# Performance work log

Hardware: AMD Instinct MI355X
Metric: run time of the kernel (lower is better)

Reference implementation:

```python
import jax, jax.numpy as jnp
import numpy as np

N, P, T, D = 25000, 100000, 4, 128
DIN = 4 * D + 4  # 516
LEAKY = 0.001


def setup_inputs() -> dict:
    key = jax.random.key(0)
    ks = jax.random.split(key, 12)
    inp = {
        "coords": jax.random.normal(ks[0], (N, T, 3), jnp.float32),
        "propers": jax.random.randint(ks[1], (P, 4), 0, N, jnp.int64),
        "encoded": jax.random.normal(ks[2], (N, D), jnp.float32),
        "t": jax.random.uniform(ks[3], (T,), jnp.float32),
        "answer": jax.random.normal(ks[4], (N, T, 3), jnp.float32),
        # AggregateMLP(516 -> 128 -> 128 -> 128 -> 2), LeakyReLU(0.001) between
        "W0": jax.random.normal(ks[5], (DIN, D), jnp.float32) / np.sqrt(DIN),
        "b0": jnp.zeros((D,), jnp.float32),
        "W1": jax.random.normal(ks[6], (D, D), jnp.float32) / np.sqrt(D),
        "b1": jnp.zeros((D,), jnp.float32),
        "W2": jax.random.normal(ks[7], (D, D), jnp.float32) / np.sqrt(D),
        "b2": jnp.zeros((D,), jnp.float32),
        "W3": jax.random.normal(ks[8], (D, 2), jnp.float32) / np.sqrt(D),
        "b3": jnp.zeros((2,), jnp.float32),
    }
    return inp


def _forward(coords, propers, encoded, t, answer, W0, b0, W1, b1, W2, b2, W3, b3):
    p0, p1, p2, p3 = propers[:, 0], propers[:, 1], propers[:, 2], propers[:, 3]
    c0, c1, c2, c3 = coords[p0], coords[p1], coords[p2], coords[p3]  # [P,T,3]
    u1 = c1 - c0
    u2 = c2 - c1
    u3 = c3 - c2
    u1xu2 = jnp.cross(u1, u2, axis=-1)
    u2xu3 = jnp.cross(u2, u3, axis=-1)
    u2_norm = jnp.linalg.norm(u2, axis=-1, keepdims=True)
    u1yu2 = u1 * u2_norm
    theta = jnp.arctan2((u1yu2 * u2xu3).sum(-1), (u1xu2 * u2xu3).sum(-1))  # [P,T]
    dr = c0 - c3  # [P,T,3]
    dl = jnp.sqrt(jnp.clip(jnp.square(dr).sum(-1), 1e-12))  # [P,T]
    dh = dr / dl[..., None]

    Pn, Tn = propers.shape[0], t.shape[0]
    bcast = lambda e: jnp.broadcast_to(e[:, None, :], (Pn, Tn, e.shape[-1]))
    feats = jnp.concatenate(
        [
            bcast(encoded[p0]),
            bcast(encoded[p1]),
            bcast(encoded[p2]),
            bcast(encoded[p3]),
            jnp.broadcast_to(t.reshape(1, Tn, 1), (Pn, Tn, 1)),
            jnp.sin(theta)[..., None],
            jnp.cos(theta)[..., None],
            dl[..., None],
        ],
        axis=2,
    )  # [P,T,516]

    h = jax.nn.leaky_relu(feats @ W0 + b0, LEAKY)
    h = jax.nn.leaky_relu(h @ W1 + b1, LEAKY)
    h = jax.nn.leaky_relu(h @ W2 + b2, LEAKY)
    delta = h @ W3 + b3  # [P,T,2]

    out = answer.at[p0].add(-0.5 * delta[:, :, 0:1] * dh)
    out = out.at[p3].add(0.5 * delta[:, :, 1:2] * dh)
    return out


def reference(coords, propers, encoded, t, answer, W0, b0, W1, b1, W2, b2, W3, b3):
    return _forward(coords, propers, encoded, t, answer, W0, b0, W1, b1, W2, b2, W3, b3)
```

## Files before the change

### kernel.cpp

```cpp
#include <hip/hip_runtime.h>
#include <hip/hip_bf16.h>

#define NN 25000
#define PP 100000
#define TT 4
#define DD 128
#define LEAKY 0.001f

#define PB 32
#define ROWS 128

typedef __bf16 bf16;
typedef __bf16 bf16x8 __attribute__((ext_vector_type(8)));
typedef float  f32x4  __attribute__((ext_vector_type(4)));

#define OFF_ENCB  0u
#define OFF_W0SW  6400000u
#define OFF_W1SW  6531072u
#define OFF_W2SW  6563840u
#define OFF_W3SW  6596608u
#define WS_END    6600704u

#define PR_ENCB4 800000
#define PR_W0SW  65536
#define PR_W1SW  16384
#define PR_W2SW  16384
#define PR_W3SW  2048
#define PR_COPY4 75000
#define PR_TOTAL (PR_ENCB4 + PR_W0SW + PR_W1SW + PR_W2SW + PR_W3SW + PR_COPY4)

__global__ __launch_bounds__(256) void prep_kernel(
    const float* __restrict__ encoded, const float* __restrict__ W0,
    const float* __restrict__ W1, const float* __restrict__ W2,
    const float* __restrict__ W3, const float* __restrict__ answer,
    bf16* __restrict__ encB, bf16* __restrict__ W0sw, bf16* __restrict__ W1sw,
    bf16* __restrict__ W2sw, bf16* __restrict__ W3sw, float* __restrict__ out)
{
    int idx = blockIdx.x * 256 + threadIdx.x;
    if (idx < PR_ENCB4) {
        float4 v = ((const float4*)encoded)[idx];
        bf16 pk[4] = {(bf16)v.x, (bf16)v.y, (bf16)v.z, (bf16)v.w};
        *(uint2*)(encB + idx * 4) = *(const uint2*)pk;
        return;
    }
    idx -= PR_ENCB4;
    if (idx < PR_W0SW) {
        int j = idx & 7, lane = (idx >> 3) & 63, c = idx >> 9;
        int fr = lane & 15, quad = lane >> 4;
        int kc = c & 15, iwv = c >> 4;
        int k = kc * 32 + quad * 8 + j;
        W0sw[idx] = (bf16)W0[k * 128 + iwv * 16 + fr];
        return;
    }
    idx -= PR_W0SW;
    if (idx < PR_W1SW) {
        int j = idx & 7, lane = (idx >> 3) & 63, c = idx >> 9;
        int fr = lane & 15, quad = lane >> 4;
        int kc = c & 3, nt = c >> 2;
        int k = kc * 32 + quad * 8 + j;
        W1sw[idx] = (bf16)W1[k * 128 + nt * 16 + fr];
        return;
    }
    idx -= PR_W1SW;
    if (idx < PR_W2SW) {
        int j = idx & 7, lane = (idx >> 3) & 63, c = idx >> 9;
        int fr = lane & 15, quad = lane >> 4;
        int kc = c & 3, nt = c >> 2;
        int k = kc * 32 + quad * 8 + j;
        W2sw[idx] = (bf16)W2[k * 128 + nt * 16 + fr];
        return;
    }
    idx -= PR_W2SW;
    if (idx < PR_W3SW) {
        int j = idx & 7, lane = (idx >> 3) & 63, kc = idx >> 9;
        int fr = lane & 15, quad = lane >> 4;
        int k = kc * 32 + quad * 8 + j;
        W3sw[idx] = (fr < 2) ? (bf16)W3[k * 2 + fr] : (bf16)0.0f;
        return;
    }
    idx -= PR_W3SW;
    if (idx < PR_COPY4) { ((float4*)out)[idx] = ((const float4*)answer)[idx]; }
}

__global__ __launch_bounds__(512, 4) void main_kernel(
    const float* __restrict__ coords, const int* __restrict__ propers,
    const float* __restrict__ tvec, const float* __restrict__ W0,
    const float* __restrict__ b0, const float* __restrict__ b1,
    const float* __restrict__ b2, const float* __restrict__ b3,
    const bf16* __restrict__ encB, const bf16* __restrict__ W0sw,
    const bf16* __restrict__ W1sw, const bf16* __restrict__ W2sw,
    const bf16* __restrict__ W3sw, float* __restrict__ out)
{
    __shared__ bf16 sBuf0[ROWS * 136];
    __shared__ bf16 sBuf1[ROWS * 136];
    #define SA(p, c)  sBuf1[(p) * 520 + (c)]
    #define SH0(r, j) sBuf0[(r) * 136 + (j)]
    #define SH1(r, j) sBuf1[(r) * 136 + (j)]
    __shared__ int   sNodes[PB][4];
    __shared__ float sSn[ROWS], sCs[ROWS], sDl[ROWS], sDh[ROWS][3];
    __shared__ float sDelta[ROWS][2];

    const int tid  = threadIdx.x;
    const int pBase = blockIdx.x * PB;
    const float tv0 = tvec[0], tv1 = tvec[1], tv2 = tvec[2], tv3 = tvec[3];

    {
        int row = tid >> 2, sg = tid & 3;
        int p = row >> 2, i = row & 3;
        int node = propers[(pBase + p) * 4 + i];
        if (sg == 0) sNodes[p][i] = node;
        const uint4* src = (const uint4*)(encB + (size_t)node * 128 + sg * 32);
        uint4* dst = (uint4*)(&SA(p, i * 128 + sg * 32));
        #pragma unroll
        for (int q = 0; q < 4; ++q) dst[q] = src[q];
    }
    if (tid < ROWS) {
        int r = tid, p = r >> 2, t = r & 3;
        const int* prow = propers + (pBase + p) * 4;
        int n0 = prow[0], n1 = prow[1], n2 = prow[2], n3 = prow[3];
        const float* c0 = coords + n0 * 12 + t * 3;
        const float* c1 = coords + n1 * 12 + t * 3;
        const float* c2 = coords + n2 * 12 + t * 3;
        const float* c3 = coords + n3 * 12 + t * 3;
        float u1x = c1[0]-c0[0], u1y = c1[1]-c0[1], u1z = c1[2]-c0[2];
        float u2x = c2[0]-c1[0], u2y = c2[1]-c1[1], u2z = c2[2]-c1[2];
        float u3x = c3[0]-c2[0], u3y = c3[1]-c2[1], u3z = c3[2]-c2[2];
        float ax = u1y*u2z - u1z*u2y, ay = u1z*u2x - u1x*u2z, az = u1x*u2y - u1y*u2x;
        float bx = u2y*u3z - u2z*u3y, by = u2z*u3x - u2x*u3z, bz = u2x*u3y - u2y*u3x;
        float u2n = sqrtf(u2x*u2x + u2y*u2y + u2z*u2z);
        float num = u2n * (u1x*bx + u1y*by + u1z*bz);
        float den = ax*bx + ay*by + az*bz;
        float hyp = sqrtf(num*num + den*den);
        float sn, cs;
        if (hyp > 1e-30f) { float ih = 1.0f / hyp; sn = num * ih; cs = den * ih; }
        else { sn = 0.0f; cs = 1.0f; }
        float drx = c0[0]-c3[0], dry = c0[1]-c3[1], drz = c0[2]-c3[2];
        float dl = sqrtf(fmaxf(drx*drx + dry*dry + drz*drz, 1e-12f));
        float il = 1.0f / dl;
        sSn[r] = sn; sCs[r] = cs; sDl[r] = dl;
        sDh[r][0] = drx * il; sDh[r][1] = dry * il; sDh[r][2] = drz * il;
    }
    __syncthreads();

    const int wv = tid >> 6, lane = tid & 63;
    const int fr = lane & 15;
    const int quad = lane >> 4;

    f32x4 acc0 = {0.f,0.f,0.f,0.f}, acc1 = {0.f,0.f,0.f,0.f};
    {
        const bf16* aB0 = &SA(fr, quad * 8);
        const bf16* aB1 = &SA(16 + fr, quad * 8);
        const bf16* w0b = W0sw + (size_t)wv * 16 * 512 + lane * 8;
        #pragma unroll
        for (int kc = 0; kc < 16; ++kc) {
            bf16x8 bF  = *(const bf16x8*)(w0b + kc * 512);
            bf16x8 aF0 = *(const bf16x8*)(aB0 + kc * 32);
            bf16x8 aF1 = *(const bf16x8*)(aB1 + kc * 32);
            acc0 = __builtin_amdgcn_mfma_f32_16x16x32_bf16(aF0, bF, acc0, 0, 0, 0);
            acc1 = __builtin_amdgcn_mfma_f32_16x16x32_bf16(aF1, bF, acc1, 0, 0, 0);
        }
    }
    {
        int j = wv * 16 + fr;
        float w512 = W0[512 * 128 + j], w513 = W0[513 * 128 + j];
        float w514 = W0[514 * 128 + j], w515 = W0[515 * 128 + j];
        float bb = b0[j];
        #pragma unroll
        for (int s = 0; s < 2; ++s) {
            const f32x4 a = s ? acc1 : acc0;
            #pragma unroll
            for (int reg = 0; reg < 4; ++reg) {
                int p = s * 16 + quad * 4 + reg;
                float g = a[reg] + bb;
                #pragma unroll
                for (int t = 0; t < 4; ++t) {
                    int r = p * 4 + t;
                    float tvv = (t == 0) ? tv0 : (t == 1) ? tv1 : (t == 2) ? tv2 : tv3;
                    float v = g + tvv * w512 + sSn[r] * w513 + sCs[r] * w514 + sDl[r] * w515;
                    v = fmaxf(v, LEAKY * v);
                    SH0(r, j) = (bf16)v;
                }
            }
        }
    }
    __syncthreads();

    const int m2 = (wv & 3) * 2;
    const int nh = wv >> 2;

    #pragma unroll
    for (int s = 0; s < 2; ++s) {
        f32x4 hacc[4];
        #pragma unroll
        for (int nt = 0; nt < 4; ++nt) hacc[nt] = (f32x4){0.f,0.f,0.f,0.f};
        const bf16* aRow = &SH0((m2 + s) * 16 + fr, quad * 8);
        const bf16* w1b = W1sw + lane * 8;
        #pragma unroll
        for (int kc = 0; kc < 4; ++kc) {
            bf16x8 aF = *(const bf16x8*)(aRow + kc * 32);
            #pragma unroll
            for (int nt = 0; nt < 4; ++nt) {
                bf16x8 bF = *(const bf16x8*)(w1b + ((nh * 4 + nt) * 4 + kc) * 512);
                hacc[nt] = __builtin_amdgcn_mfma_f32_16x16x32_bf16(aF, bF, hacc[nt], 0, 0, 0);
            }
        }
        #pragma unroll
        for (int nt = 0; nt < 4; ++nt) {
            int j = (nh * 4 + nt) * 16 + fr;
            float bb = b1[j];
            #pragma unroll
            for (int reg = 0; reg < 4; ++reg) {
                int r = (m2 + s) * 16 + quad * 4 + reg;
                float v = hacc[nt][reg] + bb;
                v = fmaxf(v, LEAKY * v);
                SH1(r, j) = (bf16)v;
            }
        }
    }
    __syncthreads();

    #pragma unroll
    for (int s = 0; s < 2; ++s) {
        f32x4 hacc[4];
        #pragma unroll
        for (int nt = 0; nt < 4; ++nt) hacc[nt] = (f32x4){0.f,0.f,0.f,0.f};
        const bf16* aRow = &SH1((m2 + s) * 16 + fr, quad * 8);
        const bf16* w2b = W2sw + lane * 8;
        #pragma unroll
        for (int kc = 0; kc < 4; ++kc) {
            bf16x8 aF = *(const bf16x8*)(aRow + kc * 32);
            #pragma unroll
            for (int nt = 0; nt < 4; ++nt) {
                bf16x8 bF = *(const bf16x8*)(w2b + ((nh * 4 + nt) * 4 + kc) * 512);
                hacc[nt] = __builtin_amdgcn_mfma_f32_16x16x32_bf16(aF, bF, hacc[nt], 0, 0, 0);
            }
        }
        #pragma unroll
        for (int nt = 0; nt < 4; ++nt) {
            int j = (nh * 4 + nt) * 16 + fr;
            float bb = b2[j];
            #pragma unroll
            for (int reg = 0; reg < 4; ++reg) {
                int r = (m2 + s) * 16 + quad * 4 + reg;
                float v = hacc[nt][reg] + bb;
                v = fmaxf(v, LEAKY * v);
                SH0(r, j) = (bf16)v;
            }
        }
    }
    __syncthreads();

    {
        f32x4 dacc = {0.f,0.f,0.f,0.f};
        const bf16* aRow = &SH0(wv * 16 + fr, quad * 8);
        const bf16* w3b = W3sw + lane * 8;
        #pragma unroll
        for (int kc = 0; kc < 4; ++kc) {
            bf16x8 aF = *(const bf16x8*)(aRow + kc * 32);
            bf16x8 bF = *(const bf16x8*)(w3b + kc * 512);
            dacc = __builtin_amdgcn_mfma_f32_16x16x32_bf16(aF, bF, dacc, 0, 0, 0);
        }
        if (fr < 2) {
            float bb = b3[fr];
            #pragma unroll
            for (int reg = 0; reg < 4; ++reg)
                sDelta[wv * 16 + quad * 4 + reg][fr] = dacc[reg] + bb;
        }
    }
    __syncthreads();

    for (int idx = tid; idx < ROWS * 6; idx += 512) {
        int r = idx / 6, c = idx % 6;
        int p = r >> 2, t = r & 3;
        int side = c / 3, ax = c % 3;
        int node = sNodes[p][side ? 3 : 0];
        float dval = side ? 0.5f * sDelta[r][1] : -0.5f * sDelta[r][0];
        atomicAdd(out + node * 12 + t * 3 + ax, dval * sDh[r][ax]);
    }
    #undef SA
    #undef SH0
    #undef SH1
}

extern "C" void kernel_launch(void* const* d_in, const int* in_sizes, int n_in,
                              void* d_out, int out_size, void* d_ws, size_t ws_size,
                              hipStream_t stream) {
    const float* coords  = (const float*)d_in[0];
    const int*   propers = (const int*)d_in[1];
    const float* encoded = (const float*)d_in[2];
    const float* tvec    = (const float*)d_in[3];
    const float* answer  = (const float*)d_in[4];
    const float* W0 = (const float*)d_in[5];
    const float* b0 = (const float*)d_in[6];
    const float* W1 = (const float*)d_in[7];
    const float* b1 = (const float*)d_in[8];
    const float* W2 = (const float*)d_in[9];
    const float* b2 = (const float*)d_in[10];
    const float* W3 = (const float*)d_in[11];
    const float* b3 = (const float*)d_in[12];
    float* out = (float*)d_out;
    char* ws = (char*)d_ws;
    bf16* encB = (bf16*)(ws + OFF_ENCB);
    bf16* W0sw = (bf16*)(ws + OFF_W0SW);
    bf16* W1sw = (bf16*)(ws + OFF_W1SW);
    bf16* W2sw = (bf16*)(ws + OFF_W2SW);
    bf16* W3sw = (bf16*)(ws + OFF_W3SW);

    int prep_blocks = (PR_TOTAL + 255) / 256;
    prep_kernel<<<prep_blocks, 256, 0, stream>>>(encoded, W0, W1, W2, W3, answer,
                                                 encB, W0sw, W1sw, W2sw, W3sw, out);
    main_kernel<<<PP / PB, 512, 0, stream>>>(coords, propers, tvec, W0, b0, b1, b2, b3,
                                             encB, W0sw, W1sw, W2sw, W3sw, out);
}
```

Measured before the change: 206.2 us.

## Precompute per-node first-layer projections and gather them instead of per-proper GEMM

The first MLP layer is linear in the four gathered embeddings, so a new kernel precomputes encoded @ W0 slice for each of the four slots per node (N×4×128 in bf16). The main kernel then gathers and sums four projected rows per proper instead of running a 512-wide K GEMM over 32 propers per block. This removes most of the layer-0 MFMA work, since it is done once per node rather than once per proper. In exchange it adds an extra kernel launch and about 25 MB of workspace writes and reads. It also introduces an extra bf16 rounding of each partial product before summation.

After: 204.9 us. No clear change (-0.6%).

```diff
diff --git a/kernel.cpp b/kernel.cpp
--- a/kernel.cpp
+++ b/kernel.cpp
@@ -19,7 +19,8 @@
 #define OFF_W1SW  6531072u
 #define OFF_W2SW  6563840u
 #define OFF_W3SW  6596608u
-#define WS_END    6600704u
+#define OFF_E     6600704u
+#define WS_END    32200704u
 
 #define PR_ENCB4 800000
 #define PR_W0SW  65536
@@ -82,18 +83,52 @@
     if (idx < PR_COPY4) { ((float4*)out)[idx] = ((const float4*)answer)[idx]; }
 }
 
+__global__ __launch_bounds__(512, 4) void prep_e_kernel(
+    const bf16* __restrict__ encB, const bf16* __restrict__ W0sw,
+    bf16* __restrict__ E)
+{
+    __shared__ bf16 sA[16][136];
+    const int tid = threadIdx.x;
+    const int row0 = blockIdx.x * 16;
+    if (tid < 256) {
+        int row = tid >> 4, seg = tid & 15;
+        int rr = row0 + row; if (rr > NN - 1) rr = NN - 1;
+        *(bf16x8*)(&sA[row][seg * 8]) =
+            *(const bf16x8*)(encB + (size_t)rr * 128 + seg * 8);
+    }
+    __syncthreads();
+    const int wv = tid >> 6, lane = tid & 63;
+    const int fr = lane & 15, quad = lane >> 4;
+    const bf16* aBase = &sA[fr][quad * 8];
+    #pragma unroll
+    for (int i = 0; i < 4; ++i) {
+        f32x4 dacc = {0.f, 0.f, 0.f, 0.f};
+        #pragma unroll
+        for (int kcc = 0; kcc < 4; ++kcc) {
+            bf16x8 aF = *(const bf16x8*)(aBase + kcc * 32);
+            bf16x8 bF = *(const bf16x8*)(W0sw + ((size_t)wv * 16 + i * 4 + kcc) * 512 + lane * 8);
+            dacc = __builtin_amdgcn_mfma_f32_16x16x32_bf16(aF, bF, dacc, 0, 0, 0);
+        }
+        #pragma unroll
+        for (int reg = 0; reg < 4; ++reg) {
+            int row = row0 + quad * 4 + reg;
+            if (row < NN)
+                E[((size_t)i * NN + row) * 128 + wv * 16 + fr] = (bf16)dacc[reg];
+        }
+    }
+}
+
 __global__ __launch_bounds__(512, 4) void main_kernel(
     const float* __restrict__ coords, const int* __restrict__ propers,
     const float* __restrict__ tvec, const float* __restrict__ W0,
     const float* __restrict__ b0, const float* __restrict__ b1,
     const float* __restrict__ b2, const float* __restrict__ b3,
-    const bf16* __restrict__ encB, const bf16* __restrict__ W0sw,
-    const bf16* __restrict__ W1sw, const bf16* __restrict__ W2sw,
-    const bf16* __restrict__ W3sw, float* __restrict__ out)
+    const bf16* __restrict__ E, const bf16* __restrict__ W1sw,
+    const bf16* __restrict__ W2sw, const bf16* __restrict__ W3sw,
+    float* __restrict__ out)
 {
     __shared__ bf16 sBuf0[ROWS * 136];
     __shared__ bf16 sBuf1[ROWS * 136];
-    #define SA(p, c)  sBuf1[(p) * 520 + (c)]
     #define SH0(r, j) sBuf0[(r) * 136 + (j)]
     #define SH1(r, j) sBuf1[(r) * 136 + (j)]
     __shared__ int   sNodes[PB][4];
@@ -104,19 +139,31 @@
     const int pBase = blockIdx.x * PB;
     const float tv0 = tvec[0], tv1 = tvec[1], tv2 = tvec[2], tv3 = tvec[3];
 
+    const int p  = tid >> 4, s8 = tid & 15;
+    bf16x8 e0, e1, e2, e3;
+    float w512v[8], w513v[8], w514v[8], w515v[8], b0v[8];
     {
-        int row = tid >> 2, sg = tid & 3;
-        int p = row >> 2, i = row & 3;
-        int node = propers[(pBase + p) * 4 + i];
-        if (sg == 0) sNodes[p][i] = node;
-        const uint4* src = (const uint4*)(encB + (size_t)node * 128 + sg * 32);
-        uint4* dst = (uint4*)(&SA(p, i * 128 + sg * 32));
-        #pragma unroll
-        for (int q = 0; q < 4; ++q) dst[q] = src[q];
-    }
+        const int* prow = propers + (pBase + p) * 4;
+        int n0 = prow[0], n1 = prow[1], n2 = prow[2], n3 = prow[3];
+        e0 = *(const bf16x8*)(E + ((size_t)0 * NN + n0) * 128 + s8 * 8);
+        e1 = *(const bf16x8*)(E + ((size_t)1 * NN + n1) * 128 + s8 * 8);
+        e2 = *(const bf16x8*)(E + ((size_t)2 * NN + n2) * 128 + s8 * 8);
+        e3 = *(const bf16x8*)(E + ((size_t)3 * NN + n3) * 128 + s8 * 8);
+        *(float4*)(w512v)     = *(const float4*)(W0 + 512 * 128 + s8 * 8);
+        *(float4*)(w512v + 4) = *(const float4*)(W0 + 512 * 128 + s8 * 8 + 4);
+        *(float4*)(w513v)     = *(const float4*)(W0 + 513 * 128 + s8 * 8);
+        *(float4*)(w513v + 4) = *(const float4*)(W0 + 513 * 128 + s8 * 8 + 4);
+        *(float4*)(w514v)     = *(const float4*)(W0 + 514 * 128 + s8 * 8);
+        *(float4*)(w514v + 4) = *(const float4*)(W0 + 514 * 128 + s8 * 8 + 4);
+        *(float4*)(w515v)     = *(const float4*)(W0 + 515 * 128 + s8 * 8);
+        *(float4*)(w515v + 4) = *(const float4*)(W0 + 515 * 128 + s8 * 8 + 4);
+        *(float4*)(b0v)       = *(const float4*)(b0 + s8 * 8);
+        *(float4*)(b0v + 4)   = *(const float4*)(b0 + s8 * 8 + 4);
+    }
+    if (tid < PB * 4) sNodes[tid >> 2][tid & 3] = propers[(pBase + (tid >> 2)) * 4 + (tid & 3)];
     if (tid < ROWS) {
-        int r = tid, p = r >> 2, t = r & 3;
-        const int* prow = propers + (pBase + p) * 4;
+        int r = tid, pp = r >> 2, t = r & 3;
+        const int* prow = propers + (pBase + pp) * 4;
         int n0 = prow[0], n1 = prow[1], n2 = prow[2], n3 = prow[3];
         const float* c0 = coords + n0 * 12 + t * 3;
         const float* c1 = coords + n1 * 12 + t * 3;
@@ -142,49 +189,30 @@
     }
     __syncthreads();
 
+    {
+        float g[8];
+        #pragma unroll
+        for (int j = 0; j < 8; ++j)
+            g[j] = (float)e0[j] + (float)e1[j] + (float)e2[j] + (float)e3[j] + b0v[j];
+        #pragma unroll
+        for (int t = 0; t < 4; ++t) {
+            int r = p * 4 + t;
+            float tvv = (t == 0) ? tv0 : (t == 1) ? tv1 : (t == 2) ? tv2 : tv3;
+            float sn = sSn[r], cs = sCs[r], dl = sDl[r];
+            bf16 hv[8];
+            #pragma unroll
+            for (int j = 0; j < 8; ++j) {
+                float v = g[j] + tvv * w512v[j] + sn * w513v[j] + cs * w514v[j] + dl * w515v[j];
+                v = fmaxf(v, LEAKY * v);
+                hv[j] = (bf16)v;
+            }
+            *(bf16x8*)(&SH0(r, s8 * 8)) = *(const bf16x8*)hv;
+        }
+    }
+    __syncthreads();
+
     const int wv = tid >> 6, lane = tid & 63;
-    const int fr = lane & 15;
-    const int quad = lane >> 4;
-
-    f32x4 acc0 = {0.f,0.f,0.f,0.f}, acc1 = {0.f,0.f,0.f,0.f};
-    {
-        const bf16* aB0 = &SA(fr, quad * 8);
-        const bf16* aB1 = &SA(16 + fr, quad * 8);
-        const bf16* w0b = W0sw + (size_t)wv * 16 * 512 + lane * 8;
-        #pragma unroll
-        for (int kc = 0; kc < 16; ++kc) {
-            bf16x8 bF  = *(const bf16x8*)(w0b + kc * 512);
-            bf16x8 aF0 = *(const bf16x8*)(aB0 + kc * 32);
-            bf16x8 aF1 = *(const bf16x8*)(aB1 + kc * 32);
-            acc0 = __builtin_amdgcn_mfma_f32_16x16x32_bf16(aF0, bF, acc0, 0, 0, 0);
-            acc1 = __builtin_amdgcn_mfma_f32_16x16x32_bf16(aF1, bF, acc1, 0, 0, 0);
-        }
-    }
-    {
-        int j = wv * 16 + fr;
-        float w512 = W0[512 * 128 + j], w513 = W0[513 * 128 + j];
-        float w514 = W0[514 * 128 + j], w515 = W0[515 * 128 + j];
-        float bb = b0[j];
-        #pragma unroll
-        for (int s = 0; s < 2; ++s) {
-            const f32x4 a = s ? acc1 : acc0;
-            #pragma unroll
-            for (int reg = 0; reg < 4; ++reg) {
-                int p = s * 16 + quad * 4 + reg;
-                float g = a[reg] + bb;
-                #pragma unroll
-                for (int t = 0; t < 4; ++t) {
-                    int r = p * 4 + t;
-                    float tvv = (t == 0) ? tv0 : (t == 1) ? tv1 : (t == 2) ? tv2 : tv3;
-                    float v = g + tvv * w512 + sSn[r] * w513 + sCs[r] * w514 + sDl[r] * w515;
-                    v = fmaxf(v, LEAKY * v);
-                    SH0(r, j) = (bf16)v;
-                }
-            }
-        }
-    }
-    __syncthreads();
-
+    const int fr = lane & 15, quad = lane >> 4;
     const int m2 = (wv & 3) * 2;
     const int nh = wv >> 2;
 
@@ -271,13 +299,12 @@
 
     for (int idx = tid; idx < ROWS * 6; idx += 512) {
         int r = idx / 6, c = idx % 6;
-        int p = r >> 2, t = r & 3;
+        int pp = r >> 2, t = r & 3;
         int side = c / 3, ax = c % 3;
-        int node = sNodes[p][side ? 3 : 0];
+        int node = sNodes[pp][side ? 3 : 0];
         float dval = side ? 0.5f * sDelta[r][1] : -0.5f * sDelta[r][0];
         atomicAdd(out + node * 12 + t * 3 + ax, dval * sDh[r][ax]);
     }
-    #undef SA
     #undef SH0
     #undef SH1
 }
@@ -305,10 +332,12 @@
     bf16* W1sw = (bf16*)(ws + OFF_W1SW);
     bf16* W2sw = (bf16*)(ws + OFF_W2SW);
     bf16* W3sw = (bf16*)(ws + OFF_W3SW);
+    bf16* E    = (bf16*)(ws + OFF_E);
 
     int prep_blocks = (PR_TOTAL + 255) / 256;
     prep_kernel<<<prep_blocks, 256, 0, stream>>>(encoded, W0, W1, W2, W3, answer,
                                                  encB, W0sw, W1sw, W2sw, W3sw, out);
+    prep_e_kernel<<<(NN + 15) / 16, 512, 0, stream>>>(encB, W0sw, E);
     main_kernel<<<PP / PB, 512, 0, stream>>>(coords, propers, tvec, W0, b0, b1, b2, b3,
-                                             encB, W0sw, W1sw, W2sw, W3sw, out);
+                                             E, W1sw, W2sw, W3sw, out);
 }
```
